# Kernel optimization log

Hardware: AMD Instinct MI355X
Metric: run time of the kernel (lower is better)

## Reference

```python
import jax, jax.numpy as jnp
import numpy as np

B, LQ, D, H, NL, NP, DFF = 8, 1800, 256, 8, 4, 4, 1024
DH = D // H
SHAPES = np.array([[100, 150], [50, 75], [25, 38], [13, 19]], dtype=np.int64)
LIN = int((SHAPES[:, 0] * SHAPES[:, 1]).sum())
QN, QP = -8.0, 7.0  # 4-bit signed LSQ


def lsq(w, alpha):
    """LSQ weight quantization (per-tensor scale, STE round/grad-scale)."""
    g = 1.0 / jnp.sqrt(w.size * QP)
    a = alpha * g + jax.lax.stop_gradient(alpha - alpha * g)  # grad-scaled alpha
    wn = jnp.clip(w / a, QN, QP)
    wq = wn + jax.lax.stop_gradient(jnp.round(wn) - wn)       # round with STE
    return wq * a


def linear_q(x, w, b, a):
    return x @ lsq(w, a).T + b


def layer_norm(x, g, b, eps=1e-5):
    m = x.mean(-1, keepdims=True)
    v = ((x - m) ** 2).mean(-1, keepdims=True)
    return (x - m) / jnp.sqrt(v + eps) * g + b


def setup_inputs():
    key = jax.random.key(0)
    ks = list(jax.random.split(key, 20))

    def nrm(i, shape, s=0.02):
        return jax.random.normal(ks[i], shape, jnp.float32) * s

    def alpha(w):
        return 2.0 * jnp.mean(jnp.abs(w)) / jnp.sqrt(QP)

    qW, kW, vW, oW = nrm(0, (D, D)), nrm(1, (D, D)), nrm(2, (D, D)), nrm(3, (D, D))
    val_W = nrm(4, (D, D))
    off_W = nrm(5, (H * NL * NP * 2, D))
    aw_W = nrm(6, (H * NL * NP, D))
    out_W = nrm(7, (D, D))
    W1, W2 = nrm(8, (DFF, D)), nrm(9, (D, DFF))
    lsi = np.concatenate([[0], np.cumsum(SHAPES[:, 0] * SHAPES[:, 1])[:-1]]).astype(np.int64)
    z = jnp.zeros
    return dict(
        tgt=nrm(10, (B, LQ, D), 1.0),
        query_pos=nrm(11, (B, LQ, D), 1.0),
        reference_points=jax.random.uniform(ks[12], (B, LQ, NL, 2), jnp.float32),
        src=nrm(13, (B, LIN, D), 1.0),
        qW=qW, qb=z(D), kW=kW, kb=z(D), vW=vW, vb=z(D), oW=oW, ob=z(D),
        a_q=alpha(qW), a_k=alpha(kW), a_v=alpha(vW), a_o=alpha(oW),
        val_W=val_W, val_b=z(D), a_val=alpha(val_W),
        off_W=off_W, off_b=z(H * NL * NP * 2),
        aw_W=aw_W, aw_b=z(H * NL * NP),
        out_W=out_W, out_b=z(D), a_out=alpha(out_W),
        W1=W1, b1=z(DFF), a_w1=alpha(W1),
        W2=W2, b2=z(D), a_w2=alpha(W2),
        ln1_g=jnp.ones(D), ln1_b=z(D),
        ln2_g=jnp.ones(D), ln2_b=z(D),
        ln3_g=jnp.ones(D), ln3_b=z(D),
        src_spatial_shapes=jnp.asarray(SHAPES),
        level_start_index=jnp.asarray(lsi),
        src_padding_mask=jnp.zeros((B, LIN), dtype=bool),
    )


def reference(tgt, query_pos, reference_points, src,
              qW, qb, kW, kb, vW, vb, oW, ob, a_q, a_k, a_v, a_o,
              val_W, val_b, a_val, off_W, off_b, aw_W, aw_b, out_W, out_b, a_out,
              W1, b1, a_w1, W2, b2, a_w2,
              ln1_g, ln1_b, ln2_g, ln2_b, ln3_g, ln3_b,
              src_spatial_shapes, level_start_index, src_padding_mask):
    shapes = np.asarray(src_spatial_shapes)  # static spatial shapes per level

    # ---- quantized self-attention (dropout = eval mode, i.e. identity) ----
    qk_in = tgt + query_pos
    q = linear_q(qk_in, qW, qb, a_q).reshape(B, LQ, H, DH)
    k = linear_q(qk_in, kW, kb, a_k).reshape(B, LQ, H, DH)
    v = linear_q(tgt, vW, vb, a_v).reshape(B, LQ, H, DH)
    scores = jnp.einsum('bqhd,bkhd->bhqk', q, k) / jnp.sqrt(jnp.float32(DH))
    p = jax.nn.softmax(scores, axis=-1)
    sa = jnp.einsum('bhqk,bkhd->bqhd', p, v).reshape(B, LQ, D)
    tgt = layer_norm(tgt + linear_q(sa, oW, ob, a_o), ln2_g, ln2_b)

    # ---- quantized multi-scale deformable cross-attention ----
    query = tgt + query_pos
    value = linear_q(src, val_W, val_b, a_val)
    value = jnp.where(src_padding_mask[..., None], 0.0, value)
    value = value.reshape(B, LIN, H, DH)
    offs = (query @ off_W.T + off_b).reshape(B, LQ, H, NL, NP, 2)
    aw = (query @ aw_W.T + aw_b).reshape(B, LQ, H, NL * NP)
    aw = jax.nn.softmax(aw, axis=-1).reshape(B, LQ, H, NL, NP)
    # offset normalizer is (W_l, H_l)
    norm = jnp.asarray(shapes[:, ::-1].astype(np.float32))  # [NL, 2]
    loc = reference_points[:, :, None, :, None, :] + offs / norm[None, None, None, :, None, :]

    bidx = jnp.arange(B)[:, None, None, None]
    hidx = jnp.arange(H)[None, None, :, None]
    acc = jnp.zeros((B, LQ, H, DH), jnp.float32)
    start = 0
    for l in range(NL):
        Hl, Wl = int(shapes[l, 0]), int(shapes[l, 1])
        v_l = jax.lax.dynamic_slice_in_dim(value, start, Hl * Wl, 1).reshape(B, Hl, Wl, H, DH)
        # grid_sample semantics: align_corners=False, zero padding
        x = loc[:, :, :, l, :, 0] * Wl - 0.5  # [B, LQ, H, NP]
        y = loc[:, :, :, l, :, 1] * Hl - 0.5
        x0 = jnp.floor(x); y0 = jnp.floor(y)
        x0i = x0.astype(jnp.int32); y0i = y0.astype(jnp.int32)
        wx1 = x - x0; wy1 = y - y0
        wx0 = 1.0 - wx1; wy0 = 1.0 - wy1

        def gather(yi, xi):
            valid = (yi >= 0) & (yi < Hl) & (xi >= 0) & (xi < Wl)
            yc = jnp.clip(yi, 0, Hl - 1); xc = jnp.clip(xi, 0, Wl - 1)
            g = v_l[bidx, yc, xc, hidx]  # [B, LQ, H, NP, DH]
            return g * valid[..., None]

        samp = (gather(y0i, x0i) * (wy0 * wx0)[..., None]
                + gather(y0i, x0i + 1) * (wy0 * wx1)[..., None]
                + gather(y0i + 1, x0i) * (wy1 * wx0)[..., None]
                + gather(y0i + 1, x0i + 1) * (wy1 * wx1)[..., None])
        acc = acc + (aw[:, :, :, l, :, None] * samp).sum(axis=3)
        start += Hl * Wl

    ca = linear_q(acc.reshape(B, LQ, D), out_W, out_b, a_out)
    tgt = layer_norm(tgt + ca, ln1_g, ln1_b)

    # ---- quantized FFN ----
    t2 = linear_q(jax.nn.relu(linear_q(tgt, W1, b1, a_w1)), W2, b2, a_w2)
    tgt = layer_norm(tgt + t2, ln3_g, ln3_b)
    return tgt
```

## Files before the change

kernel.cpp:

```cpp
#include <hip/hip_runtime.h>
#include <hip/hip_bf16.h>

static constexpr int B_   = 8;
static constexpr int LQ_  = 1800;
static constexpr int D_   = 256;
static constexpr int H_   = 8;
static constexpr int DFF_ = 1024;
static constexpr int LIN_ = 19947;
static constexpr int MQ_  = B_ * LQ_;
static constexpr int NELEM_ = MQ_ * D_;
static constexpr int PREPN_ = 1016704;

#define CDIV(a, b) (((a) + (b) - 1) / (b))

typedef unsigned short u16;
typedef unsigned int   u32;
typedef unsigned long long u64;
typedef __attribute__((ext_vector_type(8))) __bf16 bf16x8;
typedef __attribute__((ext_vector_type(4))) float  f32x4;
typedef __attribute__((ext_vector_type(4))) u32    u32x4;

#if __has_builtin(__builtin_amdgcn_exp2f)
#define EXP2(x) __builtin_amdgcn_exp2f(x)
#else
#define EXP2(x) exp2f(x)
#endif

__device__ __forceinline__ u16 f2bf(float f) {
    union { __bf16 h; u16 u; } v; v.h = (__bf16)f; return v.u;
}
__device__ __forceinline__ float bf2f(u16 u) {
    union { u32 u; float f; } v; v.u = ((u32)u) << 16;
    return v.f;
}

__device__ __forceinline__ f32x4 mfma_bf16(bf16x8 a, bf16x8 b, f32x4 c) {
    return __builtin_amdgcn_mfma_f32_16x16x32_bf16(a, b, c, 0, 0, 0);
}

__device__ __forceinline__ void gload16(const void* g, void* l) {
    __builtin_amdgcn_global_load_lds(
        (const __attribute__((address_space(1))) void*)g,
        (__attribute__((address_space(3))) void*)l,
        16, 0, 0);
}

template <int N> __device__ __forceinline__ void waitvm() {
    if constexpr (N == 0) asm volatile("s_waitcnt vmcnt(0)" ::: "memory");
    else if constexpr (N == 3) asm volatile("s_waitcnt vmcnt(3)" ::: "memory");
    else if constexpr (N == 6) asm volatile("s_waitcnt vmcnt(6)" ::: "memory");
}

__device__ __forceinline__ void storey(float* p, float v) { *p = v; }
__device__ __forceinline__ void storey(u16* p, float v)   { *p = f2bf(v); }

__global__ void k_prep(
    const float* __restrict__ qW,   const float* __restrict__ kW,
    const float* __restrict__ vW,   const float* __restrict__ oW,
    const float* __restrict__ valW, const float* __restrict__ outW,
    const float* __restrict__ W1,   const float* __restrict__ W2,
    const float* __restrict__ offW, const float* __restrict__ awW,
    const float* __restrict__ a_q,  const float* __restrict__ a_k,
    const float* __restrict__ a_v,  const float* __restrict__ a_o,
    const float* __restrict__ a_val,const float* __restrict__ a_out,
    const float* __restrict__ a_w1, const float* __restrict__ a_w2,
    const float* __restrict__ qb,   const float* __restrict__ kb,
    const float* __restrict__ off_b,const float* __restrict__ aw_b,
    const float* __restrict__ tgt,  const float* __restrict__ qpos,
    u16* __restrict__ wout, float* __restrict__ bout,
    u16* __restrict__ A, u16* __restrict__ Bb)
{
    int i = blockIdx.x * 256 + threadIdx.x;
    auto q8 = [&](const float* w, const float* al, int off) {
        float a = al[0];
        float wn = fminf(fmaxf(w[off] / a, -8.f), 7.f);
        wout[i] = f2bf(rintf(wn) * a);
    };
    if      (i <   65536) q8(qW,   a_q,   i);
    else if (i <  131072) q8(kW,   a_k,   i -   65536);
    else if (i <  196608) q8(vW,   a_v,   i -  131072);
    else if (i <  262144) q8(oW,   a_o,   i -  196608);
    else if (i <  327680) q8(valW, a_val, i -  262144);
    else if (i <  393216) q8(outW, a_out, i -  327680);
    else if (i <  655360) q8(W1,   a_w1,  i -  393216);
    else if (i <  917504) q8(W2,   a_w2,  i -  655360);
    else if (i <  983040) wout[i] = f2bf(offW[i - 917504]);
    else if (i < 1015808) wout[i] = f2bf(awW[i - 983040]);
    else if (i < 1016320) { int j = i - 1015808; bout[j]       = (j < 256) ? qb[j]    : kb[j - 256];  }
    else if (i < PREPN_)  { int j = i - 1016320; bout[512 + j] = (j < 256) ? off_b[j] : aw_b[j - 256]; }
    else {
        int j = i - PREPN_;
        if (j < NELEM_) { float t = tgt[j]; A[j] = f2bf(t + qpos[j]); Bb[j] = f2bf(t); }
    }
}

template <typename XT, typename OT, bool RELU, int BN>
__global__ __launch_bounds__(256) void k_gemm3(
    const XT* __restrict__ X, const u16* __restrict__ W,
    const float* __restrict__ bias, OT* __restrict__ Y,
    int M, int N, int K)
{
    constexpr int WN  = BN / 2;
    constexpr int NFR = WN / 16;
    constexpr bool XF32 = (sizeof(XT) == 4);
    constexpr int L = (XF32 ? 2 : 1) + BN / 64;
    constexpr int ASZ = 64 * 32 * (XF32 ? 2 : 1);
    constexpr int BSZ = BN * 32;
    __shared__ __align__(16) u16 As[2][ASZ];
    __shared__ __align__(16) u16 Bs[2][BSZ];

    const int tid = threadIdx.x;
    const int wave = tid >> 6, lane = tid & 63;
    const int wr = wave >> 1, wc = wave & 1;
    const int fr = lane & 15, fg = lane >> 4;
    const int bm = blockIdx.x * 64, bn = blockIdx.y * BN;

    f32x4 acc[2][NFR];
    #pragma unroll
    for (int m = 0; m < 2; ++m)
        #pragma unroll
        for (int n = 0; n < NFR; ++n) acc[m][n] = (f32x4){0.f, 0.f, 0.f, 0.f};

    auto stageA = [&](int buf, int kt) {
        if constexpr (!XF32) {
            int r = (wave << 4) + (lane >> 2);
            int grow = bm + r; if (grow > M - 1) grow = M - 1;
            int cs = (lane & 3) ^ ((lane >> 3) & 3);
            gload16((const u16*)X + (size_t)grow * K + (kt << 5) + (cs << 3),
                    &As[buf][wave * 512]);
        } else {
            float* Af = (float*)As[buf];
            #pragma unroll
            for (int t = 0; t < 2; ++t) {
                int r = (t << 5) + (wave << 3) + (lane >> 3);
                int grow = bm + r; if (grow > M - 1) grow = M - 1;
                int cs = (lane & 7) ^ ((lane >> 3) & 7);
                gload16((const float*)X + (size_t)grow * K + (kt << 5) + (cs << 2),
                        &Af[((t << 5) + (wave << 3)) * 32]);
            }
        }
    };
    auto stageB = [&](int buf, int kt) {
        #pragma unroll
        for (int t = 0; t < BN / 64; ++t) {
            int r = (t << 6) + (wave << 4) + (lane >> 2);
            int cs = (lane & 3) ^ ((lane >> 3) & 3);
            gload16(W + (size_t)(bn + r) * K + (kt << 5) + (cs << 3),
                    &Bs[buf][((t << 6) + (wave << 4)) * 32]);
        }
    };

    stageA(0, 0); stageB(0, 0);

    const int nk = K >> 5;
    int cur = 0;
    for (int kt = 0; kt < nk; ++kt) {
        if (kt + 1 < nk) {
            stageA(cur ^ 1, kt + 1); stageB(cur ^ 1, kt + 1);
            waitvm<L>();
        } else {
            waitvm<0>();
        }
        __builtin_amdgcn_s_barrier();

        bf16x8 af[2], bg[NFR];
        #pragma unroll
        for (int m = 0; m < 2; ++m) {
            int r = wr * 32 + m * 16 + fr;
            if constexpr (!XF32) {
                af[m] = *(const bf16x8*)&As[cur][r * 32 + ((fg ^ ((fr >> 1) & 3)) << 3)];
            } else {
                const float* Af = (const float*)As[cur];
                int s0 = (fg << 1) ^ (fr & 7);
                f32x4 x0 = *(const f32x4*)&Af[r * 32 + (s0 << 2)];
                f32x4 x1 = *(const f32x4*)&Af[r * 32 + ((s0 ^ 1) << 2)];
                #pragma unroll
                for (int j = 0; j < 4; ++j) {
                    af[m][j]     = (__bf16)x0[j];
                    af[m][4 + j] = (__bf16)x1[j];
                }
            }
        }
        #pragma unroll
        for (int n = 0; n < NFR; ++n) {
            int r = wc * WN + n * 16 + fr;
            bg[n] = *(const bf16x8*)&Bs[cur][r * 32 + ((fg ^ ((fr >> 1) & 3)) << 3)];
        }
        #pragma unroll
        for (int m = 0; m < 2; ++m)
            #pragma unroll
            for (int n = 0; n < NFR; ++n)
                acc[m][n] = mfma_bf16(af[m], bg[n], acc[m][n]);

        __builtin_amdgcn_s_barrier();
        cur ^= 1;
    }

    #pragma unroll
    for (int m = 0; m < 2; ++m) {
        #pragma unroll
        for (int i = 0; i < 4; ++i) {
            int grow = bm + wr * 32 + m * 16 + fg * 4 + i;
            if (grow >= M) continue;
            #pragma unroll
            for (int n = 0; n < NFR; ++n) {
                int gcol = bn + wc * WN + n * 16 + fr;
                float v = acc[m][n][i] + bias[gcol];
                if (RELU) v = fmaxf(v, 0.f);
                storey(Y + (size_t)grow * N + gcol, v);
            }
        }
    }
}

__global__ __launch_bounds__(256) void k_attn(
    const u16* __restrict__ QK, const u16* __restrict__ V, u16* __restrict__ O)
{
    __shared__ u16 Ks[128 * 40];
    __shared__ u16 Vt[32 * 136];
    const int b = blockIdx.z, h = blockIdx.y;
    const int q0 = blockIdx.x * 64;
    const int tid = threadIdx.x;
    const int wave = tid >> 6, lane = tid & 63;
    const int fr = lane & 15, fg = lane >> 4;
    constexpr float C2 = 0.25503486f;

    int qg = q0 + wave * 16 + fr; if (qg >= LQ_) qg = LQ_ - 1;
    bf16x8 qf;
    {
        bf16x8 qraw = *(const bf16x8*)&QK[((size_t)(b * LQ_ + qg)) * 512 + h * 32 + fg * 8];
        #pragma unroll
        for (int j = 0; j < 8; ++j) qf[j] = (__bf16)((float)qraw[j] * C2);
    }

    const bf16x8 ones = {(__bf16)1.f, (__bf16)1.f, (__bf16)1.f, (__bf16)1.f,
                         (__bf16)1.f, (__bf16)1.f, (__bf16)1.f, (__bf16)1.f};

    f32x4 o0 = (f32x4){0.f,0.f,0.f,0.f}, o1 = (f32x4){0.f,0.f,0.f,0.f};
    f32x4 lacc = (f32x4){0.f,0.f,0.f,0.f};

    const int kr = tid >> 1, kc = (tid & 1) * 16;
    const int vp = lane, vdh = wave * 8;
    const int cp = ((vp >> 4) << 4) | (((vp >> 1) & 3) << 2) | (((vp >> 3) & 1) << 1) | (vp & 1);

    for (int kb0 = 0; kb0 < LQ_; kb0 += 128) {
        const bool tail = (kb0 + 128 > LQ_);
        __syncthreads();
        {
            int kg = kb0 + kr; if (kg >= LQ_) kg = LQ_ - 1;
            const u16* kp = &QK[((size_t)(b * LQ_ + kg)) * 512 + 256 + h * 32 + kc];
            *(bf16x8*)&Ks[kr * 40 + kc]     = *(const bf16x8*)kp;
            *(bf16x8*)&Ks[kr * 40 + kc + 8] = *(const bf16x8*)(kp + 8);
            int v0 = kb0 + 2 * vp, v1 = v0 + 1;
            if (v0 >= LQ_) v0 = LQ_ - 1;
            if (v1 >= LQ_) v1 = LQ_ - 1;
            union { bf16x8 v; u16 s[8]; } va, vb2;
            va.v  = *(const bf16x8*)&V[((size_t)(b * LQ_ + v0)) * 256 + h * 32 + vdh];
            vb2.v = *(const bf16x8*)&V[((size_t)(b * LQ_ + v1)) * 256 + h * 32 + vdh];
            #pragma unroll
            for (int j = 0; j < 8; ++j)
                *(u32*)&Vt[(vdh + j) * 136 + 2 * cp] = (u32)va.s[j] | ((u32)vb2.s[j] << 16);
        }
        __syncthreads();

        u32x4 pq[4];
        #pragma unroll
        for (int f = 0; f < 8; ++f) {
            bf16x8 ka = *(const bf16x8*)&Ks[(f * 16 + fr) * 40 + fg * 8];
            f32x4 s = mfma_bf16(ka, qf, (f32x4){0.f,0.f,0.f,0.f});
            if (tail) {
                #pragma unroll
                for (int i = 0; i < 4; ++i)
                    if (kb0 + f * 16 + fg * 4 + i >= LQ_) s[i] = -3e38f;
            }
            float p0 = EXP2(s[0]), p1 = EXP2(s[1]);
            float p2 = EXP2(s[2]), p3 = EXP2(s[3]);
            union { __bf16 h[2]; u32 w; } c0, c1;
            c0.h[0] = (__bf16)p0; c0.h[1] = (__bf16)p1;
            c1.h[0] = (__bf16)p2; c1.h[1] = (__bf16)p3;
            pq[f >> 1][(f & 1) * 2 + 0] = c0.w;
            pq[f >> 1][(f & 1) * 2 + 1] = c1.w;
        }

        #pragma unroll
        for (int ks = 0; ks < 4; ++ks) {
            bf16x8 pb  = __builtin_bit_cast(bf16x8, pq[ks]);
            bf16x8 va0 = *(const bf16x8*)&Vt[fr * 136 + ks * 32 + fg * 8];
            bf16x8 va1 = *(const bf16x8*)&Vt[(16 + fr) * 136 + ks * 32 + fg * 8];
            o0 = mfma_bf16(va0, pb, o0);
            o1 = mfma_bf16(va1, pb, o1);
            lacc = mfma_bf16(ones, pb, lacc);
        }
    }

    float inv = 1.f / lacc[0];
    int qout = q0 + wave * 16 + fr;
    if (qout < LQ_) {
        size_t base = ((size_t)(b * LQ_ + qout)) * 256 + h * 32;
        #pragma unroll
        for (int i = 0; i < 4; ++i) {
            O[base + fg * 4 + i]      = f2bf(o0[i] * inv);
            O[base + 16 + fg * 4 + i] = f2bf(o1[i] * inv);
        }
    }
}

__device__ __forceinline__ float ldf(const float* p) { return *p; }
__device__ __forceinline__ float ldf(const u16* p)   { return bf2f(*p); }

template <typename RT, typename OT>
__global__ __launch_bounds__(256) void k_resln(
    const u16* __restrict__ X, const RT* __restrict__ R,
    const float* __restrict__ g, const float* __restrict__ bb,
    OT* __restrict__ O)
{
    const int row = blockIdx.x;
    const int d = threadIdx.x;
    const size_t off = (size_t)row * D_ + d;
    float v = ldf(R + off) + bf2f(X[off]);
    __shared__ float r1[4], r2[4];
    int lane = d & 63, wid = d >> 6;
    float s = v;
    #pragma unroll
    for (int o_ = 32; o_ >= 1; o_ >>= 1) s += __shfl_xor(s, o_);
    if (lane == 0) r1[wid] = s;
    __syncthreads();
    float mean = (r1[0] + r1[1] + r1[2] + r1[3]) * (1.f / 256.f);
    float dv = v - mean;
    float sq = dv * dv;
    #pragma unroll
    for (int o_ = 32; o_ >= 1; o_ >>= 1) sq += __shfl_xor(sq, o_);
    if (lane == 0) r2[wid] = sq;
    __syncthreads();
    float var = (r2[0] + r2[1] + r2[2] + r2[3]) * (1.f / 256.f);
    storey(O + off, dv / sqrtf(var + 1e-5f) * g[d] + bb[d]);
}

template <typename RT>
__global__ __launch_bounds__(256) void k_resln2(
    const u16* __restrict__ X, const RT* __restrict__ R,
    const float* __restrict__ g, const float* __restrict__ bb,
    const float* __restrict__ qpos,
    u16* __restrict__ O1, u16* __restrict__ O2)
{
    const int row = blockIdx.x;
    const int d = threadIdx.x;
    const size_t off = (size_t)row * D_ + d;
    float v = ldf(R + off) + bf2f(X[off]);
    __shared__ float r1[4], r2[4];
    int lane = d & 63, wid = d >> 6;
    float s = v;
    #pragma unroll
    for (int o_ = 32; o_ >= 1; o_ >>= 1) s += __shfl_xor(s, o_);
    if (lane == 0) r1[wid] = s;
    __syncthreads();
    float mean = (r1[0] + r1[1] + r1[2] + r1[3]) * (1.f / 256.f);
    float dv = v - mean;
    float sq = dv * dv;
    #pragma unroll
    for (int o_ = 32; o_ >= 1; o_ >>= 1) sq += __shfl_xor(sq, o_);
    if (lane == 0) r2[wid] = sq;
    __syncthreads();
    float var = (r2[0] + r2[1] + r2[2] + r2[3]) * (1.f / 256.f);
    float y = dv / sqrtf(var + 1e-5f) * g[d] + bb[d];
    O1[off] = f2bf(y);
    O2[off] = f2bf(y + qpos[off]);
}

__global__ __launch_bounds__(256) void k_sample(
    const float* __restrict__ oaw,
    const u16* __restrict__ value, const float* __restrict__ refp,
    u16* __restrict__ acc_out)
{
    __shared__ __align__(16) u32 pts[4][128][8];
    const int t = threadIdx.x;
    const int bq0 = blockIdx.x * 4;
    const int b = bq0 / LQ_;

    constexpr int Hl[4] = {100, 50, 25, 13};
    constexpr int Wl[4] = {150, 75, 38, 19};
    constexpr int LS[4] = {0, 15000, 18750, 19700};

    #pragma unroll
    for (int j = 0; j < 2; ++j) {
        const int gidx = t + j * 256;
        const int qsub = gidx >> 7;
        const int pt = gidx & 127;
        const int h = pt >> 4, lp = pt & 15;
        const int l = lp >> 2, p = lp & 3;
        const int bq = bq0 + qsub;

        float2 oxy = *(const float2*)&oaw[(size_t)bq * 384 + h * 32 + l * 8 + p * 2];
        float av = oaw[(size_t)bq * 384 + 256 + h * 16 + lp];
        float mx = av;
        #pragma unroll
        for (int s = 1; s < 16; s <<= 1) mx = fmaxf(mx, __shfl_xor(mx, s));
        float e = __expf(av - mx);
        float sum = e;
        #pragma unroll
        for (int s = 1; s < 16; s <<= 1) sum += __shfl_xor(sum, s);
        float a = e / sum;

        float2 rxy = *(const float2*)&refp[(size_t)bq * 8 + l * 2];
        const float Wf = (float)Wl[l], Hf = (float)Hl[l];
        float x = (rxy.x + oxy.x / Wf) * Wf - 0.5f;
        float y = (rxy.y + oxy.y / Hf) * Hf - 0.5f;
        float x0f = floorf(x), y0f = floorf(y);
        int x0 = (int)x0f, y0 = (int)y0f;
        float wx1 = x - x0f, wy1 = y - y0f;
        float wx0 = 1.f - wx1, wy0 = 1.f - wy1;

        u32 ov[4]; float wv[4];
        #pragma unroll
        for (int c = 0; c < 4; ++c) {
            int cy = c >> 1, cx = c & 1;
            int yi = y0 + cy, xi = x0 + cx;
            bool valid = (yi >= 0) && (yi < Hl[l]) && (xi >= 0) && (xi < Wl[l]);
            ov[c] = valid ? (u32)((LS[l] + yi * Wl[l] + xi) * 256 + h * 32) : 0u;
            float w = (cy ? wy1 : wy0) * (cx ? wx1 : wx0) * a;
            wv[c] = valid ? w : 0.f;
        }
        u32* dst = pts[qsub][lp * 8 + h];
        *(uint4*)dst = make_uint4(ov[0], ov[1], ov[2], ov[3]);
        float4 wq = make_float4(wv[0], wv[1], wv[2], wv[3]);
        *(float4*)(dst + 4) = wq;
    }
    __syncthreads();

    const int qsub = t >> 6;
    const int rem = t & 63;
    const int h = rem >> 3;
    const int dq = rem & 7;
    const u16* vb = value + (size_t)b * LIN_ * 256 + 4 * dq;
    float a0 = 0.f, a1 = 0.f, a2 = 0.f, a3 = 0.f;
    #pragma unroll
    for (int i = 0; i < 16; ++i) {
        const u32* P = pts[qsub][i * 8 + h];
        uint4 o4 = *(const uint4*)P;
        float4 w4 = *(const float4*)(P + 4);
        u64 g;
        g = *(const u64*)&vb[o4.x];
        a0 += w4.x * bf2f((u16)g);         a1 += w4.x * bf2f((u16)(g >> 16));
        a2 += w4.x * bf2f((u16)(g >> 32)); a3 += w4.x * bf2f((u16)(g >> 48));
        g = *(const u64*)&vb[o4.y];
        a0 += w4.y * bf2f((u16)g);         a1 += w4.y * bf2f((u16)(g >> 16));
        a2 += w4.y * bf2f((u16)(g >> 32)); a3 += w4.y * bf2f((u16)(g >> 48));
        g = *(const u64*)&vb[o4.z];
        a0 += w4.z * bf2f((u16)g);         a1 += w4.z * bf2f((u16)(g >> 16));
        a2 += w4.z * bf2f((u16)(g >> 32)); a3 += w4.z * bf2f((u16)(g >> 48));
        g = *(const u64*)&vb[o4.w];
        a0 += w4.w * bf2f((u16)g);         a1 += w4.w * bf2f((u16)(g >> 16));
        a2 += w4.w * bf2f((u16)(g >> 32)); a3 += w4.w * bf2f((u16)(g >> 48));
    }
    const int bq = bq0 + qsub;
    u64 packed = (u64)f2bf(a0) | ((u64)f2bf(a1) << 16)
               | ((u64)f2bf(a2) << 32) | ((u64)f2bf(a3) << 48);
    *(u64*)&acc_out[(size_t)bq * 256 + h * 32 + 4 * dq] = packed;
}

extern "C" void kernel_launch(void* const* d_in, const int* in_sizes, int n_in,
                              void* d_out, int out_size, void* d_ws, size_t ws_size,
                              hipStream_t stream)
{
    (void)in_sizes; (void)n_in; (void)out_size; (void)ws_size;
    const float* tgt   = (const float*)d_in[0];
    const float* qpos  = (const float*)d_in[1];
    const float* refp  = (const float*)d_in[2];
    const float* src   = (const float*)d_in[3];
    const float* qW    = (const float*)d_in[4];
    const float* qb    = (const float*)d_in[5];
    const float* kW    = (const float*)d_in[6];
    const float* kb    = (const float*)d_in[7];
    const float* vW    = (const float*)d_in[8];
    const float* vb    = (const float*)d_in[9];
    const float* oW    = (const float*)d_in[10];
    const float* ob    = (const float*)d_in[11];
    const float* a_q   = (const float*)d_in[12];
    const float* a_k   = (const float*)d_in[13];
    const float* a_v   = (const float*)d_in[14];
    const float* a_o   = (const float*)d_in[15];
    const float* val_W = (const float*)d_in[16];
    const float* val_b = (const float*)d_in[17];
    const float* a_val = (const float*)d_in[18];
    const float* off_W = (const float*)d_in[19];
    const float* off_b = (const float*)d_in[20];
    const float* aw_W  = (const float*)d_in[21];
    const float* aw_b  = (const float*)d_in[22];
    const float* out_W = (const float*)d_in[23];
    const float* out_b = (const float*)d_in[24];
    const float* a_out = (const float*)d_in[25];
    const float* W1    = (const float*)d_in[26];
    const float* b1    = (const float*)d_in[27];
    const float* a_w1  = (const float*)d_in[28];
    const float* W2    = (const float*)d_in[29];
    const float* b2    = (const float*)d_in[30];
    const float* a_w2  = (const float*)d_in[31];
    const float* ln1_g = (const float*)d_in[32];
    const float* ln1_b = (const float*)d_in[33];
    const float* ln2_g = (const float*)d_in[34];
    const float* ln2_b = (const float*)d_in[35];
    const float* ln3_g = (const float*)d_in[36];
    const float* ln3_b = (const float*)d_in[37];

    u16* wbase = (u16*)d_ws;
    u16* wq_q  = wbase;
    u16* wq_v  = wbase + 131072;
    u16* wq_o  = wbase + 196608;
    u16* wq_vl = wbase + 262144;
    u16* wq_ot = wbase + 327680;
    u16* wq_1  = wbase + 393216;
    u16* wq_2  = wbase + 655360;
    u16* w_off = wbase + 917504;
    float* bfused = (float*)(wbase + 1015808);
    u16* bufA = (u16*)(bfused + 1024);
    u16* bufB = bufA + NELEM_;
    u16* bufC = bufB + NELEM_;
    u16* bufD = bufC + NELEM_;
    u16* bufE = bufD + NELEM_;
    float* oaw = (float*)(bufE + NELEM_);
    u16* valb  = (u16*)(oaw + (size_t)MQ_ * 384);

    const int TB = 256;
    const int MVAL = B_ * LIN_;
    const int GM = MQ_ / 64;
    const int GV = CDIV(MVAL, 64);

    k_prep<<<CDIV(PREPN_ + NELEM_, TB), TB, 0, stream>>>(
        qW, kW, vW, oW, val_W, out_W, W1, W2, off_W, aw_W,
        a_q, a_k, a_v, a_o, a_val, a_out, a_w1, a_w2,
        qb, kb, off_b, aw_b, tgt, qpos, wbase, bfused, bufA, bufB);

    k_gemm3<u16, u16, false, 128><<<dim3(GM, 4), TB, 0, stream>>>(bufA, wq_q, bfused, bufC, MQ_, 512, 256);
    k_gemm3<u16, u16, false, 128><<<dim3(GM, 2), TB, 0, stream>>>(bufB, wq_v, vb, bufE, MQ_, 256, 256);
    k_attn<<<dim3(CDIV(LQ_,64), H_, B_), TB, 0, stream>>>(bufC, bufE, bufA);
    k_gemm3<u16, u16, false, 128><<<dim3(GM, 2), TB, 0, stream>>>(bufA, wq_o, ob, bufD, MQ_, 256, 256);
    k_resln2<float><<<MQ_, TB, 0, stream>>>(bufD, tgt, ln2_g, ln2_b, qpos, bufC, bufD);

    k_gemm3<float, u16, false, 256><<<dim3(GV, 1), TB, 0, stream>>>(src, wq_vl, val_b, valb, MVAL, 256, 256);
    k_gemm3<u16, float, false, 128><<<dim3(GM, 3), TB, 0, stream>>>(bufD, w_off, bfused + 512, oaw, MQ_, 384, 256);
    k_sample<<<MQ_ / 4, TB, 0, stream>>>(oaw, valb, refp, bufE);
    k_gemm3<u16, u16, false, 128><<<dim3(GM, 2), TB, 0, stream>>>(bufE, wq_ot, out_b, bufA, MQ_, 256, 256);
    k_resln<u16, u16><<<MQ_, TB, 0, stream>>>(bufA, bufC, ln1_g, ln1_b, bufB);

    u16* ffn1 = valb;
    k_gemm3<u16, u16, true , 128><<<dim3(GM, 8), TB, 0, stream>>>(bufB, wq_1, b1, ffn1, MQ_, 1024, 256);
    k_gemm3<u16, u16, false, 128><<<dim3(GM, 2), TB, 0, stream>>>(ffn1, wq_2, b2, bufD, MQ_, 256, 1024);
    k_resln<u16, float><<<MQ_, TB, 0, stream>>>(bufD, bufB, ln3_g, ln3_b, (float*)d_out);
}
```

Baseline: 342.3 us.

## Replace 4-wave GEMM with single-wave 64x64 tile GEMM without barriers

Replaces the 256-thread GEMM, which split a 64xBN block tile across four waves, with a 64-thread kernel where one wave computes a full 64x64 tile. That wave issues all LDS staging loads itself and runs a 4x4 grid of MFMAs per k-step. Because one wave owns its LDS buffers, the block barriers go away and the vmcnt waits are retuned to 8 or 12. The grid is reordered with N-tiles as the fast dimension so blocks sharing A rows run close together, and the attention PV MFMA loop gets a raised s_setprio. The trade-off is more blocks holding more accumulator registers each, and less sharing of B tiles across rows.

Measured after the change: 414.7 us. 1.21x slower.

```diff
diff --git a/kernel.cpp b/kernel.cpp
--- a/kernel.cpp
+++ b/kernel.cpp
@@ -46,10 +46,11 @@
 }
 
 template <int N> __device__ __forceinline__ void waitvm() {
-    if constexpr (N == 0) asm volatile("s_waitcnt vmcnt(0)" ::: "memory");
-    else if constexpr (N == 3) asm volatile("s_waitcnt vmcnt(3)" ::: "memory");
-    else if constexpr (N == 6) asm volatile("s_waitcnt vmcnt(6)" ::: "memory");
-}
+    if constexpr (N == 0)  asm volatile("s_waitcnt vmcnt(0)"  ::: "memory");
+    else if constexpr (N == 8)  asm volatile("s_waitcnt vmcnt(8)"  ::: "memory");
+    else if constexpr (N == 12) asm volatile("s_waitcnt vmcnt(12)" ::: "memory");
+}
+__device__ __forceinline__ void cfence() { asm volatile("" ::: "memory"); }
 
 __device__ __forceinline__ void storey(float* p, float v) { *p = v; }
 __device__ __forceinline__ void storey(u16* p, float v)   { *p = f2bf(v); }
@@ -94,63 +95,65 @@
     }
 }
 
-template <typename XT, typename OT, bool RELU, int BN>
-__global__ __launch_bounds__(256) void k_gemm3(
+template <typename XT, typename OT, bool RELU>
+__global__ __launch_bounds__(64) void k_gemm5(
     const XT* __restrict__ X, const u16* __restrict__ W,
     const float* __restrict__ bias, OT* __restrict__ Y,
     int M, int N, int K)
 {
-    constexpr int WN  = BN / 2;
-    constexpr int NFR = WN / 16;
     constexpr bool XF32 = (sizeof(XT) == 4);
-    constexpr int L = (XF32 ? 2 : 1) + BN / 64;
+    constexpr int LA = XF32 ? 8 : 4;
+    constexpr int LB = 4;
+    constexpr int L  = LA + LB;
     constexpr int ASZ = 64 * 32 * (XF32 ? 2 : 1);
-    constexpr int BSZ = BN * 32;
     __shared__ __align__(16) u16 As[2][ASZ];
-    __shared__ __align__(16) u16 Bs[2][BSZ];
-
-    const int tid = threadIdx.x;
-    const int wave = tid >> 6, lane = tid & 63;
-    const int wr = wave >> 1, wc = wave & 1;
+    __shared__ __align__(16) u16 Bs[2][64 * 32];
+
+    const int lane = threadIdx.x;
     const int fr = lane & 15, fg = lane >> 4;
-    const int bm = blockIdx.x * 64, bn = blockIdx.y * BN;
-
-    f32x4 acc[2][NFR];
-    #pragma unroll
-    for (int m = 0; m < 2; ++m)
-        #pragma unroll
-        for (int n = 0; n < NFR; ++n) acc[m][n] = (f32x4){0.f, 0.f, 0.f, 0.f};
+    const int bm = blockIdx.y * 64, bn = blockIdx.x * 64;
 
     auto stageA = [&](int buf, int kt) {
         if constexpr (!XF32) {
-            int r = (wave << 4) + (lane >> 2);
-            int grow = bm + r; if (grow > M - 1) grow = M - 1;
-            int cs = (lane & 3) ^ ((lane >> 3) & 3);
-            gload16((const u16*)X + (size_t)grow * K + (kt << 5) + (cs << 3),
-                    &As[buf][wave * 512]);
+            const int u  = lane >> 2;
+            const int cs = (lane & 3) ^ ((lane >> 3) & 3);
+            #pragma unroll
+            for (int t = 0; t < 4; ++t) {
+                int grow = bm + t * 16 + u; if (grow > M - 1) grow = M - 1;
+                gload16((const u16*)X + (size_t)grow * K + (kt << 5) + (cs << 3),
+                        &As[buf][t * 512]);
+            }
         } else {
             float* Af = (float*)As[buf];
+            const int u  = lane >> 3;
+            const int cs = (lane & 7) ^ ((lane >> 3) & 7);
             #pragma unroll
-            for (int t = 0; t < 2; ++t) {
-                int r = (t << 5) + (wave << 3) + (lane >> 3);
-                int grow = bm + r; if (grow > M - 1) grow = M - 1;
-                int cs = (lane & 7) ^ ((lane >> 3) & 7);
+            for (int t = 0; t < 8; ++t) {
+                int grow = bm + t * 8 + u; if (grow > M - 1) grow = M - 1;
                 gload16((const float*)X + (size_t)grow * K + (kt << 5) + (cs << 2),
-                        &Af[((t << 5) + (wave << 3)) * 32]);
+                        &Af[t * 256]);
             }
         }
     };
     auto stageB = [&](int buf, int kt) {
-        #pragma unroll
-        for (int t = 0; t < BN / 64; ++t) {
-            int r = (t << 6) + (wave << 4) + (lane >> 2);
-            int cs = (lane & 3) ^ ((lane >> 3) & 3);
-            gload16(W + (size_t)(bn + r) * K + (kt << 5) + (cs << 3),
-                    &Bs[buf][((t << 6) + (wave << 4)) * 32]);
+        const int u  = lane >> 2;
+        const int cs = (lane & 3) ^ ((lane >> 3) & 3);
+        #pragma unroll
+        for (int t = 0; t < 4; ++t) {
+            int r = bn + t * 16 + u;
+            gload16(W + (size_t)r * K + (kt << 5) + (cs << 3),
+                    &Bs[buf][t * 512]);
         }
     };
 
+    f32x4 acc[4][4];
+    #pragma unroll
+    for (int m = 0; m < 4; ++m)
+        #pragma unroll
+        for (int n = 0; n < 4; ++n) acc[m][n] = (f32x4){0.f, 0.f, 0.f, 0.f};
+
     stageA(0, 0); stageB(0, 0);
+    cfence();
 
     const int nk = K >> 5;
     int cur = 0;
@@ -161,12 +164,11 @@
         } else {
             waitvm<0>();
         }
-        __builtin_amdgcn_s_barrier();
-
-        bf16x8 af[2], bg[NFR];
-        #pragma unroll
-        for (int m = 0; m < 2; ++m) {
-            int r = wr * 32 + m * 16 + fr;
+
+        bf16x8 af[4], bg[4];
+        #pragma unroll
+        for (int m = 0; m < 4; ++m) {
+            int r = m * 16 + fr;
             if constexpr (!XF32) {
                 af[m] = *(const bf16x8*)&As[cur][r * 32 + ((fg ^ ((fr >> 1) & 3)) << 3)];
             } else {
@@ -182,29 +184,27 @@
             }
         }
         #pragma unroll
-        for (int n = 0; n < NFR; ++n) {
-            int r = wc * WN + n * 16 + fr;
-            bg[n] = *(const bf16x8*)&Bs[cur][r * 32 + ((fg ^ ((fr >> 1) & 3)) << 3)];
-        }
-        #pragma unroll
-        for (int m = 0; m < 2; ++m)
+        for (int n = 0; n < 4; ++n)
+            bg[n] = *(const bf16x8*)&Bs[cur][(n * 16 + fr) * 32 + ((fg ^ ((fr >> 1) & 3)) << 3)];
+
+        #pragma unroll
+        for (int m = 0; m < 4; ++m)
             #pragma unroll
-            for (int n = 0; n < NFR; ++n)
+            for (int n = 0; n < 4; ++n)
                 acc[m][n] = mfma_bf16(af[m], bg[n], acc[m][n]);
 
-        __builtin_amdgcn_s_barrier();
         cur ^= 1;
     }
 
     #pragma unroll
-    for (int m = 0; m < 2; ++m) {
+    for (int m = 0; m < 4; ++m) {
         #pragma unroll
         for (int i = 0; i < 4; ++i) {
-            int grow = bm + wr * 32 + m * 16 + fg * 4 + i;
+            int grow = bm + m * 16 + fg * 4 + i;
             if (grow >= M) continue;
             #pragma unroll
-            for (int n = 0; n < NFR; ++n) {
-                int gcol = bn + wc * WN + n * 16 + fr;
+            for (int n = 0; n < 4; ++n) {
+                int gcol = bn + n * 16 + fr;
                 float v = acc[m][n][i] + bias[gcol];
                 if (RELU) v = fmaxf(v, 0.f);
                 storey(Y + (size_t)grow * N + gcol, v);
@@ -282,6 +282,7 @@
             pq[f >> 1][(f & 1) * 2 + 1] = c1.w;
         }
 
+        __builtin_amdgcn_s_setprio(1);
         #pragma unroll
         for (int ks = 0; ks < 4; ++ks) {
             bf16x8 pb  = __builtin_bit_cast(bf16x8, pq[ks]);
@@ -291,6 +292,7 @@
             o1 = mfma_bf16(va1, pb, o1);
             lacc = mfma_bf16(ones, pb, lacc);
         }
+        __builtin_amdgcn_s_setprio(0);
     }
 
     float inv = 1.f / lacc[0];
@@ -530,20 +532,20 @@
         a_q, a_k, a_v, a_o, a_val, a_out, a_w1, a_w2,
         qb, kb, off_b, aw_b, tgt, qpos, wbase, bfused, bufA, bufB);
 
-    k_gemm3<u16, u16, false, 128><<<dim3(GM, 4), TB, 0, stream>>>(bufA, wq_q, bfused, bufC, MQ_, 512, 256);
-    k_gemm3<u16, u16, false, 128><<<dim3(GM, 2), TB, 0, stream>>>(bufB, wq_v, vb, bufE, MQ_, 256, 256);
+    k_gemm5<u16, u16, false><<<dim3(8, GM), 64, 0, stream>>>(bufA, wq_q, bfused, bufC, MQ_, 512, 256);
+    k_gemm5<u16, u16, false><<<dim3(4, GM), 64, 0, stream>>>(bufB, wq_v, vb, bufE, MQ_, 256, 256);
     k_attn<<<dim3(CDIV(LQ_,64), H_, B_), TB, 0, stream>>>(bufC, bufE, bufA);
-    k_gemm3<u16, u16, false, 128><<<dim3(GM, 2), TB, 0, stream>>>(bufA, wq_o, ob, bufD, MQ_, 256, 256);
+    k_gemm5<u16, u16, false><<<dim3(4, GM), 64, 0, stream>>>(bufA, wq_o, ob, bufD, MQ_, 256, 256);
     k_resln2<float><<<MQ_, TB, 0, stream>>>(bufD, tgt, ln2_g, ln2_b, qpos, bufC, bufD);
 
-    k_gemm3<float, u16, false, 256><<<dim3(GV, 1), TB, 0, stream>>>(src, wq_vl, val_b, valb, MVAL, 256, 256);
-    k_gemm3<u16, float, false, 128><<<dim3(GM, 3), TB, 0, stream>>>(bufD, w_off, bfused + 512, oaw, MQ_, 384, 256);
+    k_gemm5<float, u16, false><<<dim3(4, GV), 64, 0, stream>>>(src, wq_vl, val_b, valb, MVAL, 256, 256);
+    k_gemm5<u16, float, false><<<dim3(6, GM), 64, 0, stream>>>(bufD, w_off, bfused + 512, oaw, MQ_, 384, 256);
     k_sample<<<MQ_ / 4, TB, 0, stream>>>(oaw, valb, refp, bufE);
-    k_gemm3<u16, u16, false, 128><<<dim3(GM, 2), TB, 0, stream>>>(bufE, wq_ot, out_b, bufA, MQ_, 256, 256);
+    k_gemm5<u16, u16, false><<<dim3(4, GM), 64, 0, stream>>>(bufE, wq_ot, out_b, bufA, MQ_, 256, 256);
     k_resln<u16, u16><<<MQ_, TB, 0, stream>>>(bufA, bufC, ln1_g, ln1_b, bufB);
 
     u16* ffn1 = valb;
-    k_gemm3<u16, u16, true , 128><<<dim3(GM, 8), TB, 0, stream>>>(bufB, wq_1, b1, ffn1, MQ_, 1024, 256);
-    k_gemm3<u16, u16, false, 128><<<dim3(GM, 2), TB, 0, stream>>>(ffn1, wq_2, b2, bufD, MQ_, 256, 1024);
+    k_gemm5<u16, u16, true ><<<dim3(16, GM), 64, 0, stream>>>(bufB, wq_1, b1, ffn1, MQ_, 1024, 256);
+    k_gemm5<u16, u16, false><<<dim3(4, GM), 64, 0, stream>>>(ffn1, wq_2, b2, bufD, MQ_, 256, 1024);
     k_resln<u16, float><<<MQ_, TB, 0, stream>>>(bufD, bufB, ln3_g, ln3_b, (float*)d_out);
 }
```
